# Performance work log

Measured on AMD Instinct MI355X. Metric: run time of the kernel, lower is better.

The kernel has to match this reference:

```python
import jax, jax.numpy as jnp
import numpy as np

B, N, H = 8, 256, 128


def _linear_params(key, fin, fout):
    # torch nn.Linear default init: U(-1/sqrt(fin), 1/sqrt(fin)) for weight and bias
    k1, k2 = jax.random.split(key)
    lim = 1.0 / np.sqrt(fin)
    w = jax.random.uniform(k1, (fin, fout), jnp.float32, -lim, lim)
    b = jax.random.uniform(k2, (fout,), jnp.float32, -lim, lim)
    return w, b


def setup_inputs() -> dict:
    key = jax.random.key(0)
    ks = jax.random.split(key, 12)
    inp = {
        'x': jax.random.normal(ks[0], (B, N, 3), jnp.float32),
        'h': jax.random.normal(ks[1], (B, N, H), jnp.float32),
        'x0': jax.random.normal(ks[2], (B, N, 3), jnp.float32),
        'pad_mask': jnp.ones((B, N, 1), jnp.float32),
    }
    names_dims = [
        ('edg1', 2 * H + 2, H), ('edg2', H, H), ('edgi', H, 1),
        ('node1', 2 * H, H), ('node2', H, H),
        ('cor1', 2 * H + 2, H), ('cor2', H, H), ('cor3', H, 1),
    ]
    for i, (name, fin, fout) in enumerate(names_dims):
        w, b = _linear_params(ks[3 + i], fin, fout)
        inp[name + '_w'] = w
        inp[name + '_b'] = b
    return inp


def _safe_dist(d2):
    # sqrt with zero (not NaN) gradient where d2 == 0 (diagonal)
    pos = d2 > 0
    return jnp.sqrt(jnp.where(pos, d2, 1.0)) * pos


def reference(x, h, x0, pad_mask,
              edg1_w, edg1_b, edg2_w, edg2_b, edgi_w, edgi_b,
              node1_w, node1_b, node2_w, node2_b,
              cor1_w, cor1_b, cor2_w, cor2_b, cor3_w, cor3_b):
    silu = jax.nn.silu
    b, n, hd = h.shape
    # pairwise squared distances, shapes (b, n, n, 1)
    diff0 = x0[:, :, None, :] - x0[:, None, :, :]
    d0_2 = jnp.sum(diff0 * diff0, axis=-1, keepdims=True)
    diff = x[:, :, None, :] - x[:, None, :, :]
    d2 = jnp.sum(diff * diff, axis=-1, keepdims=True)
    dist = _safe_dist(d2)
    # all-pairs node-feature concat: pair[b,i,j] = [h_i, h_j, d2_ij, d0_2_ij]
    hi = jnp.broadcast_to(h[:, :, None, :], (b, n, n, hd))
    hj = jnp.broadcast_to(h[:, None, :, :], (b, n, n, hd))
    pair = jnp.concatenate([hi, hj, d2, d0_2], axis=-1)  # (b,n,n,2H+2)
    # edge MLP -> messages
    m = silu(silu(pair @ edg1_w + edg1_b) @ edg2_w + edg2_b)  # (b,n,n,H)
    e = jax.nn.sigmoid(m @ edgi_w + edgi_b)                   # (b,n,n,1)
    offdiag = 1.0 - jnp.eye(n, dtype=x.dtype)[None, :, :, None]
    e = e * offdiag
    agg = jnp.mean(e * m, axis=2)  # mean over j -> (b,n,H)
    # node update with residual
    nin = jnp.concatenate([h, agg], axis=-1)
    h_next = h + (silu(nin @ node1_w + node1_b) @ node2_w + node2_b)
    # coordinate update
    cw = silu(silu(pair @ cor1_w + cor1_b) @ cor2_w + cor2_b) @ cor3_w + cor3_b  # (b,n,n,1)
    shift = diff / (dist + 1.0)
    upd = jnp.mean(cw * shift * offdiag, axis=2)  # (b,n,3)
    x_next = x + upd
    if pad_mask is not None:
        x_next = x_next * pad_mask
        h_next = h_next * pad_mask
    return x_next, h_next
```

## Files before the change

kernel.cpp:

```cpp
#include <hip/hip_runtime.h>

typedef __attribute__((ext_vector_type(8))) short short8;
typedef __attribute__((ext_vector_type(8))) unsigned short ushort8_t;
typedef __attribute__((ext_vector_type(4))) float f32x4;

#define BN 256
#define HD 128
#define WSTRIDE 136

__device__ __forceinline__ unsigned short f2bf(float f) {
    union { float f; unsigned int i; } v; v.f = f;
    unsigned int lsb = (v.i >> 16) & 1u;
    v.i += 0x7fffu + lsb;
    return (unsigned short)(v.i >> 16);
}
__device__ __forceinline__ float fsigmoid(float x) {
    return __builtin_amdgcn_rcpf(1.0f + __expf(-x));
}
__device__ __forceinline__ float fsilu(float x) {
    return x * fsigmoid(x);
}

__global__ __launch_bounds__(256) void prep_tw(const float* __restrict__ e2w,
                                               const float* __restrict__ c2w,
                                               const float* __restrict__ e1w,
                                               const float* __restrict__ c1w,
                                               unsigned short* __restrict__ WtE,
                                               unsigned short* __restrict__ WtC,
                                               unsigned short* __restrict__ W1e1,
                                               unsigned short* __restrict__ W1e2,
                                               unsigned short* __restrict__ W1c1,
                                               unsigned short* __restrict__ W1c2) {
    int k = blockIdx.x;
    int t = threadIdx.x;
    int n = t & 127;
    if (t < 128) {
        WtE [n * 128 + k] = f2bf(e2w[k * 128 + n]);
        W1e1[n * 128 + k] = f2bf(e1w[k * 128 + n]);
        W1e2[n * 128 + k] = f2bf(e1w[(128 + k) * 128 + n]);
    } else {
        WtC [n * 128 + k] = f2bf(c2w[k * 128 + n]);
        W1c1[n * 128 + k] = f2bf(c1w[k * 128 + n]);
        W1c2[n * 128 + k] = f2bf(c1w[(128 + k) * 128 + n]);
    }
}

__global__ __launch_bounds__(256) void prep_gemm(
    const float* __restrict__ h,
    const unsigned short* __restrict__ W1e1, const unsigned short* __restrict__ W1e2,
    const unsigned short* __restrict__ W1c1, const unsigned short* __restrict__ W1c2,
    const float* __restrict__ e1b, const float* __restrict__ c1b,
    float* __restrict__ A1e, float* __restrict__ A2e,
    float* __restrict__ A1c, float* __restrict__ A2c) {
    const int tid = threadIdx.x;
    const int lane = tid & 63, wv = tid >> 6;
    const int c = lane & 15, q = lane >> 4;
    const int r0 = blockIdx.x * 16;

    const unsigned short* Wt = (wv == 0) ? W1e1 : (wv == 1) ? W1e2 : (wv == 2) ? W1c1 : W1c2;
    float* O = (wv == 0) ? A1e : (wv == 1) ? A2e : (wv == 2) ? A1c : A2c;
    const float* bias = (wv == 0) ? e1b : (wv == 2) ? c1b : (const float*)0;

    f32x4 acc[8];
    const f32x4 zf = {0.f, 0.f, 0.f, 0.f};
#pragma unroll
    for (int nt = 0; nt < 8; ++nt) acc[nt] = zf;

    const float* hrow = h + (size_t)(r0 + c) * HD;
#pragma unroll
    for (int ks = 0; ks < 4; ++ks) {
        const int kb = ks * 32 + q * 8;
        float4 hlo = *(const float4*)(hrow + kb);
        float4 hhi = *(const float4*)(hrow + kb + 4);
        short8 af;
        af[0] = (short)f2bf(hlo.x); af[1] = (short)f2bf(hlo.y);
        af[2] = (short)f2bf(hlo.z); af[3] = (short)f2bf(hlo.w);
        af[4] = (short)f2bf(hhi.x); af[5] = (short)f2bf(hhi.y);
        af[6] = (short)f2bf(hhi.z); af[7] = (short)f2bf(hhi.w);
#pragma unroll
        for (int nt = 0; nt < 8; ++nt) {
            short8 Bf = *(const short8*)(Wt + (nt * 16 + c) * HD + kb);
            acc[nt] = __builtin_amdgcn_mfma_f32_16x16x32_bf16(af, Bf, acc[nt], 0, 0, 0);
        }
    }
#pragma unroll
    for (int nt = 0; nt < 8; ++nt) {
        float bb = bias ? bias[nt * 16 + c] : 0.f;
#pragma unroll
        for (int reg = 0; reg < 4; ++reg)
            O[(size_t)(r0 + q * 4 + reg) * HD + nt * 16 + c] = acc[nt][reg] + bb;
    }
}

__global__ __launch_bounds__(1024, 8) void egc_main(
    const float* __restrict__ x, const float* __restrict__ h,
    const float* __restrict__ x0, const float* __restrict__ pmask,
    const float* __restrict__ e1w,
    const float* __restrict__ e2b, const float* __restrict__ eiw,
    const float* __restrict__ eib,
    const float* __restrict__ n1w, const float* __restrict__ n1b,
    const float* __restrict__ n2w, const float* __restrict__ n2b,
    const float* __restrict__ c1w, const float* __restrict__ c2b,
    const float* __restrict__ c3w, const float* __restrict__ c3b,
    const float* __restrict__ A1e, const float* __restrict__ A2e,
    const float* __restrict__ A1c, const float* __restrict__ A2c,
    const unsigned short* __restrict__ WtE, const unsigned short* __restrict__ WtC,
    float* __restrict__ xout, float* __restrict__ hout) {

    __shared__ __align__(16) unsigned short Wl[HD * WSTRIDE];
    __shared__ __align__(16) float xs[BN][4];
    __shared__ __align__(16) float x0s[BN][4];
    __shared__ __align__(16) float d2s[BN], d02s[BN], rsh[BN];
    __shared__ __align__(16) float vE0[HD], vE1[HD], vE2[HD];
    __shared__ __align__(16) float vC0[HD], vC1[HD], vC2[HD];
    __shared__ __align__(16) float hsv[HD];
    __shared__ __align__(16) float aggbuf[16][HD];
    __shared__ __align__(16) float aggv[HD];
    __shared__ float updbuf[16][4];
    __shared__ float smask;

    const int tid = threadIdx.x;
    const int bi  = blockIdx.x;
    const int b   = bi >> 8;
    const int i   = bi & 255;
    const int row = bi;

#pragma unroll
    for (int u = 0; u < 2; ++u) {
        int idx = u * 1024 + tid;
        int n   = idx >> 4;
        int k8  = (idx & 15) * 8;
        *(ushort8_t*)(Wl + n * WSTRIDE + k8) = *(const ushort8_t*)(WtE + n * HD + k8);
    }

    if (tid < BN) {
        int gj = b * BN + tid;
        xs[tid][0]  = x[gj * 3 + 0];
        xs[tid][1]  = x[gj * 3 + 1];
        xs[tid][2]  = x[gj * 3 + 2];
        x0s[tid][0] = x0[gj * 3 + 0];
        x0s[tid][1] = x0[gj * 3 + 1];
        x0s[tid][2] = x0[gj * 3 + 2];
    } else if (tid < BN + HD) {
        int t = tid - BN;
        vE0[t] = A1e[row * HD + t];
        vE1[t] = e1w[256 * HD + t];
        vE2[t] = e1w[257 * HD + t];
    } else if (tid < BN + 2 * HD) {
        int t = tid - BN - HD;
        vC0[t] = A1c[row * HD + t];
        vC1[t] = c1w[256 * HD + t];
        vC2[t] = c1w[257 * HD + t];
    } else if (tid < BN + 3 * HD) {
        int t = tid - BN - 2 * HD;
        hsv[t] = h[row * HD + t];
    }
    if (tid == 1023) smask = pmask[row];
    __syncthreads();

    if (tid < BN) {
        float dx = xs[i][0] - xs[tid][0];
        float dy = xs[i][1] - xs[tid][1];
        float dz = xs[i][2] - xs[tid][2];
        float d2 = dx * dx + dy * dy + dz * dz;
        d2s[tid] = d2;
        float dist = (d2 > 0.0f) ? sqrtf(d2) : 0.0f;
        rsh[tid] = __builtin_amdgcn_rcpf(dist + 1.0f);
        float ex = x0s[i][0] - x0s[tid][0];
        float ey = x0s[i][1] - x0s[tid][1];
        float ez = x0s[i][2] - x0s[tid][2];
        d02s[tid] = ex * ex + ey * ey + ez * ez;
    }
    __syncthreads();

    const int lane = tid & 63, wv = tid >> 6;
    const int c = lane & 15, q = lane >> 4;
    const int ra = wv * 16 + c;

    {
        const float* A2g = A2e + (size_t)b * BN * HD;
        f32x4 acc[8];
        const f32x4 zf = {0.f, 0.f, 0.f, 0.f};
#pragma unroll
        for (int nt = 0; nt < 8; ++nt) acc[nt] = zf;
        const float d2v = d2s[ra], d02v = d02s[ra];
#pragma unroll
        for (int ks = 0; ks < 4; ++ks) {
            const int kb = ks * 32 + q * 8;
            float4 alo = *(const float4*)(A2g + ra * HD + kb);
            float4 ahi = *(const float4*)(A2g + ra * HD + kb + 4);
            float4 p0 = *(const float4*)(vE0 + kb);
            float4 p0h = *(const float4*)(vE0 + kb + 4);
            float4 p1 = *(const float4*)(vE1 + kb);
            float4 p1h = *(const float4*)(vE1 + kb + 4);
            float4 p2 = *(const float4*)(vE2 + kb);
            float4 p2h = *(const float4*)(vE2 + kb + 4);
            short8 af;
            af[0] = (short)f2bf(fsilu(alo.x + p0.x + d2v * p1.x + d02v * p2.x));
            af[1] = (short)f2bf(fsilu(alo.y + p0.y + d2v * p1.y + d02v * p2.y));
            af[2] = (short)f2bf(fsilu(alo.z + p0.z + d2v * p1.z + d02v * p2.z));
            af[3] = (short)f2bf(fsilu(alo.w + p0.w + d2v * p1.w + d02v * p2.w));
            af[4] = (short)f2bf(fsilu(ahi.x + p0h.x + d2v * p1h.x + d02v * p2h.x));
            af[5] = (short)f2bf(fsilu(ahi.y + p0h.y + d2v * p1h.y + d02v * p2h.y));
            af[6] = (short)f2bf(fsilu(ahi.z + p0h.z + d2v * p1h.z + d02v * p2h.z));
            af[7] = (short)f2bf(fsilu(ahi.w + p0h.w + d2v * p1h.w + d02v * p2h.w));
#pragma unroll
            for (int nt = 0; nt < 8; ++nt) {
                short8 Bf = *(const short8*)(Wl + (nt * 16 + c) * WSTRIDE + kb);
                acc[nt] = __builtin_amdgcn_mfma_f32_16x16x32_bf16(af, Bf, acc[nt], 0, 0, 0);
            }
        }
        float b2l[8], wIl[8];
#pragma unroll
        for (int nt = 0; nt < 8; ++nt) {
            b2l[nt] = e2b[nt * 16 + c];
            wIl[nt] = eiw[nt * 16 + c];
        }
        float bI = eib[0];
        float aggp[8] = {0,0,0,0,0,0,0,0};
#pragma unroll
        for (int reg = 0; reg < 4; ++reg) {
            int r = wv * 16 + q * 4 + reg;
            float mv[8]; float ed = 0.f;
#pragma unroll
            for (int nt = 0; nt < 8; ++nt) {
                mv[nt] = fsilu(acc[nt][reg] + b2l[nt]);
                ed += mv[nt] * wIl[nt];
            }
            ed += __shfl_xor(ed, 1);
            ed += __shfl_xor(ed, 2);
            ed += __shfl_xor(ed, 4);
            ed += __shfl_xor(ed, 8);
            float e = (r == i) ? 0.0f : fsigmoid(ed + bI);
#pragma unroll
            for (int nt = 0; nt < 8; ++nt) aggp[nt] += e * mv[nt];
        }
#pragma unroll
        for (int nt = 0; nt < 8; ++nt) {
            aggp[nt] += __shfl_xor(aggp[nt], 16);
            aggp[nt] += __shfl_xor(aggp[nt], 32);
        }
        if (q == 0)
#pragma unroll
            for (int nt = 0; nt < 8; ++nt) aggbuf[wv][nt * 16 + c] = aggp[nt];
    }
    __syncthreads();

    if (tid < HD) {
        float s = 0.f;
#pragma unroll
        for (int w = 0; w < 16; ++w) s += aggbuf[w][tid];
        aggv[tid] = s * (1.0f / 256.0f);
    }
#pragma unroll
    for (int u = 0; u < 2; ++u) {
        int idx = u * 1024 + tid;
        int n   = idx >> 4;
        int k8  = (idx & 15) * 8;
        *(ushort8_t*)(Wl + n * WSTRIDE + k8) = *(const ushort8_t*)(WtC + n * HD + k8);
    }
    __syncthreads();

    {
        const float* A2g = A2c + (size_t)b * BN * HD;
        f32x4 acc[8];
        const f32x4 zf = {0.f, 0.f, 0.f, 0.f};
#pragma unroll
        for (int nt = 0; nt < 8; ++nt) acc[nt] = zf;
        const float d2v = d2s[ra], d02v = d02s[ra];
#pragma unroll
        for (int ks = 0; ks < 4; ++ks) {
            const int kb = ks * 32 + q * 8;
            float4 alo = *(const float4*)(A2g + ra * HD + kb);
            float4 ahi = *(const float4*)(A2g + ra * HD + kb + 4);
            float4 p0 = *(const float4*)(vC0 + kb);
            float4 p0h = *(const float4*)(vC0 + kb + 4);
            float4 p1 = *(const float4*)(vC1 + kb);
            float4 p1h = *(const float4*)(vC1 + kb + 4);
            float4 p2 = *(const float4*)(vC2 + kb);
            float4 p2h = *(const float4*)(vC2 + kb + 4);
            short8 af;
            af[0] = (short)f2bf(fsilu(alo.x + p0.x + d2v * p1.x + d02v * p2.x));
            af[1] = (short)f2bf(fsilu(alo.y + p0.y + d2v * p1.y + d02v * p2.y));
            af[2] = (short)f2bf(fsilu(alo.z + p0.z + d2v * p1.z + d02v * p2.z));
            af[3] = (short)f2bf(fsilu(alo.w + p0.w + d2v * p1.w + d02v * p2.w));
            af[4] = (short)f2bf(fsilu(ahi.x + p0h.x + d2v * p1h.x + d02v * p2h.x));
            af[5] = (short)f2bf(fsilu(ahi.y + p0h.y + d2v * p1h.y + d02v * p2h.y));
            af[6] = (short)f2bf(fsilu(ahi.z + p0h.z + d2v * p1h.z + d02v * p2h.z));
            af[7] = (short)f2bf(fsilu(ahi.w + p0h.w + d2v * p1h.w + d02v * p2h.w));
#pragma unroll
            for (int nt = 0; nt < 8; ++nt) {
                short8 Bf = *(const short8*)(Wl + (nt * 16 + c) * WSTRIDE + kb);
                acc[nt] = __builtin_amdgcn_mfma_f32_16x16x32_bf16(af, Bf, acc[nt], 0, 0, 0);
            }
        }
        float b2l[8], w3l[8];
#pragma unroll
        for (int nt = 0; nt < 8; ++nt) {
            b2l[nt] = c2b[nt * 16 + c];
            w3l[nt] = c3w[nt * 16 + c];
        }
        float b3 = c3b[0];
        float updp = 0.f;
        float xic = (c < 3) ? xs[i][c] : 0.f;
#pragma unroll
        for (int reg = 0; reg < 4; ++reg) {
            int r = wv * 16 + q * 4 + reg;
            float cd = 0.f;
#pragma unroll
            for (int nt = 0; nt < 8; ++nt)
                cd += fsilu(acc[nt][reg] + b2l[nt]) * w3l[nt];
            cd += __shfl_xor(cd, 1);
            cd += __shfl_xor(cd, 2);
            cd += __shfl_xor(cd, 4);
            cd += __shfl_xor(cd, 8);
            float cw = cd + b3;
            if (c < 3 && r != i)
                updp += cw * (xic - xs[r][c]) * rsh[r];
        }
        updp += __shfl_xor(updp, 16);
        updp += __shfl_xor(updp, 32);
        if (q == 0 && c < 3) updbuf[wv][c] = updp;
    }
    __syncthreads();

    if (tid < 3) {
        float u = 0.f;
#pragma unroll
        for (int w = 0; w < 16; ++w) u += updbuf[w][tid];
        u *= (1.0f / 256.0f);
        xout[row * 3 + tid] = (xs[i][tid] + u) * smask;
    }

    float* npart = &aggbuf[0][0];
    float* qv    = &aggbuf[8][0];
    {
        int k = tid & 127, part = tid >> 7;
        const float* src = (part < 4) ? hsv : aggv;
        int fbase = (part & 3) * 32;
        int wrow = ((part < 4) ? 0 : HD) + fbase;
        float s = 0.f;
#pragma unroll 4
        for (int f = 0; f < 32; ++f)
            s += src[fbase + f] * n1w[(size_t)(wrow + f) * HD + k];
        npart[part * HD + k] = s;
    }
    __syncthreads();
    if (tid < HD) {
        float s = n1b[tid];
#pragma unroll
        for (int p = 0; p < 8; ++p) s += npart[p * HD + tid];
        qv[tid] = fsilu(s);
    }
    __syncthreads();
    {
        int o = tid & 127, p = tid >> 7;
        float s = 0.f;
#pragma unroll 4
        for (int f = 0; f < 16; ++f) {
            int ff = p * 16 + f;
            s += qv[ff] * n2w[(size_t)ff * HD + o];
        }
        npart[p * HD + o] = s;
    }
    __syncthreads();
    if (tid < HD) {
        float s = 0.f;
#pragma unroll
        for (int p = 0; p < 8; ++p) s += npart[p * HD + tid];
        hout[(size_t)row * HD + tid] = (hsv[tid] + s + n2b[tid]) * smask;
    }
}

extern "C" void kernel_launch(void* const* d_in, const int* in_sizes, int n_in,
                              void* d_out, int out_size, void* d_ws, size_t ws_size,
                              hipStream_t stream) {
    const float* x    = (const float*)d_in[0];
    const float* h    = (const float*)d_in[1];
    const float* x0   = (const float*)d_in[2];
    const float* pm   = (const float*)d_in[3];
    const float* e1w  = (const float*)d_in[4];
    const float* e1b  = (const float*)d_in[5];
    const float* e2w  = (const float*)d_in[6];
    const float* e2b  = (const float*)d_in[7];
    const float* eiw  = (const float*)d_in[8];
    const float* eib  = (const float*)d_in[9];
    const float* n1w  = (const float*)d_in[10];
    const float* n1b  = (const float*)d_in[11];
    const float* n2w  = (const float*)d_in[12];
    const float* n2b  = (const float*)d_in[13];
    const float* c1w  = (const float*)d_in[14];
    const float* c1b  = (const float*)d_in[15];
    const float* c2w  = (const float*)d_in[16];
    const float* c2b  = (const float*)d_in[17];
    const float* c3w  = (const float*)d_in[18];
    const float* c3b  = (const float*)d_in[19];

    float* wsf = (float*)d_ws;
    const size_t nA = 2048 * 128;
    float* A1e = wsf;
    float* A2e = wsf + nA;
    float* A1c = wsf + 2 * nA;
    float* A2c = wsf + 3 * nA;
    unsigned short* WtE  = (unsigned short*)(wsf + 4 * nA);
    unsigned short* WtC  = WtE  + 128 * 128;
    unsigned short* W1e1 = WtC  + 128 * 128;
    unsigned short* W1e2 = W1e1 + 128 * 128;
    unsigned short* W1c1 = W1e2 + 128 * 128;
    unsigned short* W1c2 = W1c1 + 128 * 128;

    float* xout = (float*)d_out;
    float* hout = xout + 8 * 256 * 3;

    prep_tw<<<dim3(128), dim3(256), 0, stream>>>(e2w, c2w, e1w, c1w,
                                                 WtE, WtC, W1e1, W1e2, W1c1, W1c2);
    prep_gemm<<<dim3(128), dim3(256), 0, stream>>>(h, W1e1, W1e2, W1c1, W1c2,
                                                   e1b, c1b, A1e, A2e, A1c, A2c);
    egc_main<<<dim3(2048), dim3(1024), 0, stream>>>(
        x, h, x0, pm, e1w, e2b, eiw, eib, n1w, n1b, n2w, n2b,
        c1w, c2b, c3w, c3b, A1e, A2e, A1c, A2c, WtE, WtC, xout, hout);
}
```

Before: 221.9 us.

## Use cheaper bf16 packing, LDS-tiled weight transpose, and shared bias staging

Replaces round-to-nearest-even bf16 conversion with a simpler add-and-truncate rounding and packs pairs of values with a single perm instruction, cutting the VALU work in the main kernel's activation-to-MFMA path. The weight transpose prep kernel now uses 6 blocks that transpose through LDS with vectorized stores, instead of 128 blocks doing strided scalar writes. Small bias and weight vectors are staged in shared memory once per block rather than loaded from global memory per lane. The rounding change alters numerics slightly, since ties are no longer rounded to even.

```diff
diff --git a/kernel.cpp b/kernel.cpp
--- a/kernel.cpp
+++ b/kernel.cpp
@@ -3,16 +3,19 @@
 typedef __attribute__((ext_vector_type(8))) short short8;
 typedef __attribute__((ext_vector_type(8))) unsigned short ushort8_t;
 typedef __attribute__((ext_vector_type(4))) float f32x4;
+typedef __attribute__((ext_vector_type(4))) unsigned int uint4v;
 
 #define BN 256
 #define HD 128
 #define WSTRIDE 136
 
 __device__ __forceinline__ unsigned short f2bf(float f) {
-    union { float f; unsigned int i; } v; v.f = f;
-    unsigned int lsb = (v.i >> 16) & 1u;
-    v.i += 0x7fffu + lsb;
-    return (unsigned short)(v.i >> 16);
+    return (unsigned short)((__float_as_uint(f) + 0x8000u) >> 16);
+}
+__device__ __forceinline__ unsigned int pk2bf(float lo, float hi) {
+    unsigned int a = __float_as_uint(lo) + 0x8000u;
+    unsigned int b = __float_as_uint(hi) + 0x8000u;
+    return __builtin_amdgcn_perm(b, a, 0x07060302);
 }
 __device__ __forceinline__ float fsigmoid(float x) {
     return __builtin_amdgcn_rcpf(1.0f + __expf(-x));
@@ -21,27 +24,40 @@
     return x * fsigmoid(x);
 }
 
-__global__ __launch_bounds__(256) void prep_tw(const float* __restrict__ e2w,
-                                               const float* __restrict__ c2w,
-                                               const float* __restrict__ e1w,
-                                               const float* __restrict__ c1w,
-                                               unsigned short* __restrict__ WtE,
-                                               unsigned short* __restrict__ WtC,
-                                               unsigned short* __restrict__ W1e1,
-                                               unsigned short* __restrict__ W1e2,
-                                               unsigned short* __restrict__ W1c1,
-                                               unsigned short* __restrict__ W1c2) {
-    int k = blockIdx.x;
-    int t = threadIdx.x;
-    int n = t & 127;
-    if (t < 128) {
-        WtE [n * 128 + k] = f2bf(e2w[k * 128 + n]);
-        W1e1[n * 128 + k] = f2bf(e1w[k * 128 + n]);
-        W1e2[n * 128 + k] = f2bf(e1w[(128 + k) * 128 + n]);
-    } else {
-        WtC [n * 128 + k] = f2bf(c2w[k * 128 + n]);
-        W1c1[n * 128 + k] = f2bf(c1w[k * 128 + n]);
-        W1c2[n * 128 + k] = f2bf(c1w[(128 + k) * 128 + n]);
+__global__ __launch_bounds__(1024) void prep_tw(const float* __restrict__ e2w,
+                                                const float* __restrict__ c2w,
+                                                const float* __restrict__ e1w,
+                                                const float* __restrict__ c1w,
+                                                unsigned short* __restrict__ WtE,
+                                                unsigned short* __restrict__ WtC,
+                                                unsigned short* __restrict__ W1e1,
+                                                unsigned short* __restrict__ W1e2,
+                                                unsigned short* __restrict__ W1c1,
+                                                unsigned short* __restrict__ W1c2) {
+    __shared__ unsigned short lt[128][130];
+    const int m = blockIdx.x;
+    const float* src = (m == 0) ? e2w : (m == 1) ? c2w : (m == 2) ? e1w :
+                       (m == 3) ? (e1w + 128 * 128) : (m == 4) ? c1w : (c1w + 128 * 128);
+    unsigned short* dst = (m == 0) ? WtE : (m == 1) ? WtC : (m == 2) ? W1e1 :
+                          (m == 3) ? W1e2 : (m == 4) ? W1c1 : W1c2;
+    const int tid = threadIdx.x;
+    {
+        int k  = tid >> 3;
+        int c0 = (tid & 7) * 16;
+        const float* sp = src + k * 128 + c0;
+#pragma unroll
+        for (int j = 0; j < 16; ++j)
+            lt[c0 + j][k] = f2bf(sp[j]);
+    }
+    __syncthreads();
+    {
+        int n  = tid >> 3;
+        int k8 = (tid & 7) * 16;
+        ushort8_t o0, o1;
+#pragma unroll
+        for (int j = 0; j < 8; ++j) { o0[j] = lt[n][k8 + j]; o1[j] = lt[n][k8 + 8 + j]; }
+        *(ushort8_t*)(dst + n * 128 + k8)     = o0;
+        *(ushort8_t*)(dst + n * 128 + k8 + 8) = o1;
     }
 }
 
@@ -72,11 +88,10 @@
         const int kb = ks * 32 + q * 8;
         float4 hlo = *(const float4*)(hrow + kb);
         float4 hhi = *(const float4*)(hrow + kb + 4);
-        short8 af;
-        af[0] = (short)f2bf(hlo.x); af[1] = (short)f2bf(hlo.y);
-        af[2] = (short)f2bf(hlo.z); af[3] = (short)f2bf(hlo.w);
-        af[4] = (short)f2bf(hhi.x); af[5] = (short)f2bf(hhi.y);
-        af[6] = (short)f2bf(hhi.z); af[7] = (short)f2bf(hhi.w);
+        uint4v u;
+        u.x = pk2bf(hlo.x, hlo.y); u.y = pk2bf(hlo.z, hlo.w);
+        u.z = pk2bf(hhi.x, hhi.y); u.w = pk2bf(hhi.z, hhi.w);
+        short8 af = __builtin_bit_cast(short8, u);
 #pragma unroll
         for (int nt = 0; nt < 8; ++nt) {
             short8 Bf = *(const short8*)(Wt + (nt * 16 + c) * HD + kb);
@@ -114,6 +129,7 @@
     __shared__ __align__(16) float vE0[HD], vE1[HD], vE2[HD];
     __shared__ __align__(16) float vC0[HD], vC1[HD], vC2[HD];
     __shared__ __align__(16) float hsv[HD];
+    __shared__ __align__(16) float sE2b[HD], sEiw[HD], sC2b[HD], sC3w[HD];
     __shared__ __align__(16) float aggbuf[16][HD];
     __shared__ __align__(16) float aggv[HD];
     __shared__ float updbuf[16][4];
@@ -154,6 +170,12 @@
     } else if (tid < BN + 3 * HD) {
         int t = tid - BN - 2 * HD;
         hsv[t] = h[row * HD + t];
+    } else if (tid < BN + 4 * HD) {
+        int t = tid - BN - 3 * HD;
+        sE2b[t] = e2b[t];
+        sEiw[t] = eiw[t];
+        sC2b[t] = c2b[t];
+        sC3w[t] = c3w[t];
     }
     if (tid == 1023) smask = pmask[row];
     __syncthreads();
@@ -195,15 +217,18 @@
             float4 p1h = *(const float4*)(vE1 + kb + 4);
             float4 p2 = *(const float4*)(vE2 + kb);
             float4 p2h = *(const float4*)(vE2 + kb + 4);
-            short8 af;
-            af[0] = (short)f2bf(fsilu(alo.x + p0.x + d2v * p1.x + d02v * p2.x));
-            af[1] = (short)f2bf(fsilu(alo.y + p0.y + d2v * p1.y + d02v * p2.y));
-            af[2] = (short)f2bf(fsilu(alo.z + p0.z + d2v * p1.z + d02v * p2.z));
-            af[3] = (short)f2bf(fsilu(alo.w + p0.w + d2v * p1.w + d02v * p2.w));
-            af[4] = (short)f2bf(fsilu(ahi.x + p0h.x + d2v * p1h.x + d02v * p2h.x));
-            af[5] = (short)f2bf(fsilu(ahi.y + p0h.y + d2v * p1h.y + d02v * p2h.y));
-            af[6] = (short)f2bf(fsilu(ahi.z + p0h.z + d2v * p1h.z + d02v * p2h.z));
-            af[7] = (short)f2bf(fsilu(ahi.w + p0h.w + d2v * p1h.w + d02v * p2h.w));
+            float a0 = fsilu(alo.x + p0.x + d2v * p1.x + d02v * p2.x);
+            float a1 = fsilu(alo.y + p0.y + d2v * p1.y + d02v * p2.y);
+            float a2 = fsilu(alo.z + p0.z + d2v * p1.z + d02v * p2.z);
+            float a3 = fsilu(alo.w + p0.w + d2v * p1.w + d02v * p2.w);
+            float a4 = fsilu(ahi.x + p0h.x + d2v * p1h.x + d02v * p2h.x);
+            float a5 = fsilu(ahi.y + p0h.y + d2v * p1h.y + d02v * p2h.y);
+            float a6 = fsilu(ahi.z + p0h.z + d2v * p1h.z + d02v * p2h.z);
+            float a7 = fsilu(ahi.w + p0h.w + d2v * p1h.w + d02v * p2h.w);
+            uint4v u;
+            u.x = pk2bf(a0, a1); u.y = pk2bf(a2, a3);
+            u.z = pk2bf(a4, a5); u.w = pk2bf(a6, a7);
+            short8 af = __builtin_bit_cast(short8, u);
 #pragma unroll
             for (int nt = 0; nt < 8; ++nt) {
                 short8 Bf = *(const short8*)(Wl + (nt * 16 + c) * WSTRIDE + kb);
@@ -213,8 +238,8 @@
         float b2l[8], wIl[8];
 #pragma unroll
         for (int nt = 0; nt < 8; ++nt) {
-            b2l[nt] = e2b[nt * 16 + c];
-            wIl[nt] = eiw[nt * 16 + c];
+            b2l[nt] = sE2b[nt * 16 + c];
+            wIl[nt] = sEiw[nt * 16 + c];
         }
         float bI = eib[0];
         float aggp[8] = {0,0,0,0,0,0,0,0};
@@ -279,15 +304,18 @@
             float4 p1h = *(const float4*)(vC1 + kb + 4);
             float4 p2 = *(const float4*)(vC2 + kb);
             float4 p2h = *(const float4*)(vC2 + kb + 4);
-            short8 af;
-            af[0] = (short)f2bf(fsilu(alo.x + p0.x + d2v * p1.x + d02v * p2.x));
-            af[1] = (short)f2bf(fsilu(alo.y + p0.y + d2v * p1.y + d02v * p2.y));
-            af[2] = (short)f2bf(fsilu(alo.z + p0.z + d2v * p1.z + d02v * p2.z));
-            af[3] = (short)f2bf(fsilu(alo.w + p0.w + d2v * p1.w + d02v * p2.w));
-            af[4] = (short)f2bf(fsilu(ahi.x + p0h.x + d2v * p1h.x + d02v * p2h.x));
-            af[5] = (short)f2bf(fsilu(ahi.y + p0h.y + d2v * p1h.y + d02v * p2h.y));
-            af[6] = (short)f2bf(fsilu(ahi.z + p0h.z + d2v * p1h.z + d02v * p2h.z));
-            af[7] = (short)f2bf(fsilu(ahi.w + p0h.w + d2v * p1h.w + d02v * p2h.w));
+            float a0 = fsilu(alo.x + p0.x + d2v * p1.x + d02v * p2.x);
+            float a1 = fsilu(alo.y + p0.y + d2v * p1.y + d02v * p2.y);
+            float a2 = fsilu(alo.z + p0.z + d2v * p1.z + d02v * p2.z);
+            float a3 = fsilu(alo.w + p0.w + d2v * p1.w + d02v * p2.w);
+            float a4 = fsilu(ahi.x + p0h.x + d2v * p1h.x + d02v * p2h.x);
+            float a5 = fsilu(ahi.y + p0h.y + d2v * p1h.y + d02v * p2h.y);
+            float a6 = fsilu(ahi.z + p0h.z + d2v * p1h.z + d02v * p2h.z);
+            float a7 = fsilu(ahi.w + p0h.w + d2v * p1h.w + d02v * p2h.w);
+            uint4v u;
+            u.x = pk2bf(a0, a1); u.y = pk2bf(a2, a3);
+            u.z = pk2bf(a4, a5); u.w = pk2bf(a6, a7);
+            short8 af = __builtin_bit_cast(short8, u);
 #pragma unroll
             for (int nt = 0; nt < 8; ++nt) {
                 short8 Bf = *(const short8*)(Wl + (nt * 16 + c) * WSTRIDE + kb);
@@ -297,8 +325,8 @@
         float b2l[8], w3l[8];
 #pragma unroll
         for (int nt = 0; nt < 8; ++nt) {
-            b2l[nt] = c2b[nt * 16 + c];
-            w3l[nt] = c3w[nt * 16 + c];
+            b2l[nt] = sC2b[nt * 16 + c];
+            w3l[nt] = sC3w[nt * 16 + c];
         }
         float b3 = c3b[0];
         float updp = 0.f;
@@ -412,8 +440,8 @@
     float* xout = (float*)d_out;
     float* hout = xout + 8 * 256 * 3;
 
-    prep_tw<<<dim3(128), dim3(256), 0, stream>>>(e2w, c2w, e1w, c1w,
-                                                 WtE, WtC, W1e1, W1e2, W1c1, W1c2);
+    prep_tw<<<dim3(6), dim3(1024), 0, stream>>>(e2w, c2w, e1w, c1w,
+                                                WtE, WtC, W1e1, W1e2, W1c1, W1c2);
     prep_gemm<<<dim3(128), dim3(256), 0, stream>>>(h, W1e1, W1e2, W1c1, W1c2,
                                                    e1b, c1b, A1e, A2e, A1c, A2c);
     egc_main<<<dim3(2048), dim3(1024), 0, stream>>>(
```

Result: slower. 336.9 us (+51.9%).
